# Optimization experiments

Hardware: AMD Instinct MI355X
Metric: run time of the kernel (lower is better)

Reference implementation:

```python
import jax, jax.numpy as jnp
import numpy as np

EPS = 1e-5


def gather_nodes(nodes, idx):
    # nodes: [B,N,C], idx: [B,N,K] -> [B,N,K,C]
    return jax.vmap(lambda n, e: n[e])(nodes, idx)


def layer_norm(x, g, b):
    m = jnp.mean(x, axis=-1, keepdims=True)
    v = jnp.mean((x - m) ** 2, axis=-1, keepdims=True)
    return (x - m) * jax.lax.rsqrt(v + EPS) * g + b


def linear(x, W, b):
    return x @ W + b


def setup_inputs() -> dict:
    key = jax.random.key(0)
    B, N, K, H = 2, 2048, 48, 128
    ks = jax.random.split(key, 32)
    it = iter(range(32))
    def nrm(shape, scale=0.05):
        return jax.random.normal(ks[next(it)], shape, dtype=jnp.float32) * scale
    inp = {
        "h_V": nrm((B, N, H), 1.0),
        "h_V_atom": nrm((B, N, H), 1.0),
        "h_E": nrm((B, N, K, H), 1.0),
        # message MLP 1: in = H + 2*(H+H) = 5H = 640
        "W1": nrm((5 * H, H)), "b1": jnp.zeros((H,), jnp.float32),
        "W2": nrm((H, H)), "b2": jnp.zeros((H,), jnp.float32),
        "W3": nrm((H, H)), "b3": jnp.zeros((H,), jnp.float32),
        # message MLP 2: in = H + (H+H) = 3H = 384
        "W11": nrm((3 * H, H)), "b11": jnp.zeros((H,), jnp.float32),
        "W12": nrm((H, H)), "b12": jnp.zeros((H,), jnp.float32),
        "W13": nrm((H, H)), "b13": jnp.zeros((H,), jnp.float32),
        # FFN
        "W_in": nrm((H, 4 * H)), "b_in": jnp.zeros((4 * H,), jnp.float32),
        "W_out": nrm((4 * H, H)), "b_out": jnp.zeros((H,), jnp.float32),
        # LayerNorms
        "g1": jnp.ones((H,), jnp.float32), "be1": jnp.zeros((H,), jnp.float32),
        "g2": jnp.ones((H,), jnp.float32), "be2": jnp.zeros((H,), jnp.float32),
        "g3": jnp.ones((H,), jnp.float32), "be3": jnp.zeros((H,), jnp.float32),
        "mask_V": jnp.ones((B, N), jnp.float32),
        "mask_attend": jnp.ones((B, N, K), jnp.float32),
        "E_idx": jax.random.randint(ks[next(it)], (B, N, K), 0, N),
    }
    return inp


def reference(h_V, h_V_atom, h_E, W1, b1, W2, b2, W3, b3, W11, b11, W12, b12,
              W13, b13, W_in, b_in, W_out, b_out, g1, be1, g2, be2, g3, be3,
              mask_V, mask_attend, E_idx):
    gelu = lambda x: jax.nn.gelu(x, approximate=False)
    SCALE = 30.0
    K = h_E.shape[-2]

    # --- node message ---
    h_EV = jnp.concatenate([
        jnp.broadcast_to(h_V[:, :, None, :], h_E.shape[:3] + (h_V.shape[-1],)),
        h_E, gather_nodes(h_V, E_idx),
        h_E, gather_nodes(h_V_atom, E_idx),
    ], axis=-1)  # [B,N,K,5H]
    h_message = linear(gelu(linear(gelu(linear(h_EV, W1, b1)), W2, b2)), W3, b3)
    h_message = mask_attend[..., None] * h_message
    dh = jnp.sum(h_message, axis=-2) / SCALE
    h_V = layer_norm(h_V + dh, g1, be1)

    # --- FFN ---
    dh = linear(gelu(linear(h_V, W_in, b_in)), W_out, b_out)
    h_V = layer_norm(h_V + dh, g2, be2)
    h_V = mask_V[..., None] * h_V

    # --- edge update ---
    h_EV2 = jnp.concatenate([
        jnp.broadcast_to(h_V[:, :, None, :], h_E.shape[:3] + (h_V.shape[-1],)),
        h_E, gather_nodes(h_V, E_idx),
    ], axis=-1)  # [B,N,K,3H]
    h_message = linear(gelu(linear(gelu(linear(h_EV2, W11, b11)), W12, b12)), W13, b13)
    h_E = layer_norm(h_E + h_message, g3, be3)
    return (h_V, h_E)
```

## Files before the change

kernel.cpp:

```cpp
#include <hip/hip_runtime.h>
#include <hip/hip_bf16.h>

#define H 128
#define NN 2048
#define BB 2
#define EPSF 1e-5f

typedef __bf16 bf16;
typedef bf16 bf16x8 __attribute__((ext_vector_type(8)));
typedef bf16 bf16x4 __attribute__((ext_vector_type(4)));
typedef float f32x4 __attribute__((ext_vector_type(4)));

#define U1_F     155648
#define U2_F     679936
#define HVMID_F  1204224
#define HVMID_B  3457024
#define HV2_B    3981312
#define HV_B     4505600
#define HVA_B    5029888

__device__ __forceinline__ float gelu_f(float x) {
    float u = x * x;
    float p = __builtin_fmaf(u, 0.044715f, 1.0f);
    float w = x * p;
    float e = __builtin_amdgcn_exp2f(w * -2.3022083f);
    return x * __builtin_amdgcn_rcpf(1.0f + e);
}

#define MFMA16(a, b, c) __builtin_amdgcn_mfma_f32_16x16x32_bf16((a), (b), (c), 0, 0, 0)

#define GEMM_PIPE(U, A_EXPR, B0p, B1p, ACC)                                       \
    {                                                                             \
        bf16x8 bq0[3], bq1[3];                                                    \
        _Pragma("unroll")                                                         \
        for (int j = 0; j < 3 && j < (U); ++j) {                                  \
            bq0[j] = *(const bf16x8*)((B0p) + j * 32);                            \
            bq1[j] = *(const bf16x8*)((B1p) + j * 32);                            \
        }                                                                         \
        bf16x8 afc[3], afn[3];                                                    \
        _Pragma("unroll")                                                         \
        for (int rt = 0; rt < 3; ++rt) { const int u = 0; afc[rt] = (A_EXPR); }   \
        _Pragma("unroll")                                                         \
        for (int uu = 0; uu < (U); ++uu) {                                        \
            if (uu + 1 < (U)) {                                                   \
                _Pragma("unroll")                                                 \
                for (int rt = 0; rt < 3; ++rt) { const int u = uu + 1; afn[rt] = (A_EXPR); } \
            }                                                                     \
            __builtin_amdgcn_s_setprio(1);                                        \
            _Pragma("unroll")                                                     \
            for (int rt = 0; rt < 3; ++rt) {                                      \
                ACC[rt][0] = MFMA16(afc[rt], bq0[uu % 3], ACC[rt][0]);            \
                ACC[rt][1] = MFMA16(afc[rt], bq1[uu % 3], ACC[rt][1]);            \
            }                                                                     \
            __builtin_amdgcn_s_setprio(0);                                        \
            if (uu + 3 < (U)) {                                                   \
                bq0[uu % 3] = *(const bf16x8*)((B0p) + (uu + 3) * 32);            \
                bq1[uu % 3] = *(const bf16x8*)((B1p) + (uu + 3) * 32);            \
            }                                                                     \
            _Pragma("unroll")                                                     \
            for (int rt = 0; rt < 3; ++rt) afc[rt] = afn[rt];                     \
        }                                                                         \
    }

#define PACK_STORE(DST, ROW, PCOL, V0, V1)                                        \
    {                                                                             \
        union { bf16 h[2]; unsigned u; } pk_;                                     \
        pk_.h[0] = (V0); pk_.h[1] = (V1);                                         \
        *(unsigned*)&DST[ROW][PCOL] = pk_.u;                                      \
    }

__global__ void prep_weights(const float* __restrict__ W1, const float* __restrict__ W2,
                             const float* __restrict__ W3, const float* __restrict__ W11,
                             const float* __restrict__ W12, const float* __restrict__ W13,
                             const float* __restrict__ Win, const float* __restrict__ Wout,
                             bf16* __restrict__ ws)
{
    int i = blockIdx.x * 256 + threadIdx.x;
    float v;
    if (i < 65536) {
        int c = i >> 9, k = i & 511, s = k >> 7, k0 = k & 127;
        if (s == 0)      v = W1[k0 * H + c];
        else if (s == 1) v = W1[(128 + k0) * H + c] + W1[(384 + k0) * H + c];
        else if (s == 2) v = W1[(256 + k0) * H + c];
        else             v = W1[(512 + k0) * H + c];
    } else if (i < 81920)  { int j = i - 65536;  int c = j >> 7, p = j & 127;
                             int k = (p & ~31) + ((p & 1) << 4) + ((p & 31) >> 1);
                             v = W2[k * H + c]; }
    else if (i < 98304)    { int j = i - 81920;  int c = j >> 7, p = j & 127;
                             int k = (p & ~31) + ((p & 1) << 4) + ((p & 31) >> 1);
                             v = W3[k * H + c]; }
    else if (i < 147456)   { int j = i - 98304;  int c = j / 384, k = j - c * 384; v = W11[k * H + c]; }
    else if (i < 163840)   { int j = i - 147456; int c = j >> 7, p = j & 127;
                             int k = (p & ~31) + ((p & 1) << 4) + ((p & 31) >> 1);
                             v = W12[k * H + c]; }
    else if (i < 180224)   { int j = i - 163840; int c = j >> 7, p = j & 127;
                             int k = (p & ~31) + ((p & 1) << 4) + ((p & 31) >> 1);
                             v = W13[k * H + c]; }
    else if (i < 245760)   { int j = i - 180224; int jj = j >> 7, k = j & 127; v = Win[k * 512 + jj]; }
    else                   { int j = i - 245760; int c = j >> 9, k = j & 511; v = Wout[k * H + c]; }
    ws[i] = (bf16)v;
}

__global__ __launch_bounds__(512) void u1_kernel(
    const float* __restrict__ hV, const float* __restrict__ hVa,
    const float* __restrict__ b1, bf16* __restrict__ ws, float* __restrict__ wsf)
{
    int n0 = blockIdx.x * 128;
    int t = threadIdx.x, w = t >> 6, l = t & 63, l16 = l & 15, lg = l >> 4;
    int wm = w >> 2, wn = w & 3;
    __shared__ __align__(16) bf16 sA[128][136];

    #pragma unroll
    for (int i = 0; i < 8; ++i) {
        int idx = t + i * 512;
        int row = idx >> 5, c4 = (idx & 31) << 2;
        f32x4 v = *(const f32x4*)(hV + (size_t)(n0 + row) * H + c4);
        bf16x4 o; o[0] = (bf16)v[0]; o[1] = (bf16)v[1]; o[2] = (bf16)v[2]; o[3] = (bf16)v[3];
        *(bf16x4*)(&sA[row][c4]) = o;
        *(bf16x4*)(ws + HV_B + (size_t)(n0 + row) * H + c4) = o;
        f32x4 va = *(const f32x4*)(hVa + (size_t)(n0 + row) * H + c4);
        bf16x4 oa; oa[0] = (bf16)va[0]; oa[1] = (bf16)va[1]; oa[2] = (bf16)va[2]; oa[3] = (bf16)va[3];
        *(bf16x4*)(ws + HVA_B + (size_t)(n0 + row) * H + c4) = oa;
    }
    __syncthreads();

    f32x4 acc[4][2];
    #pragma unroll
    for (int rt = 0; rt < 4; ++rt)
        #pragma unroll
        for (int c2 = 0; c2 < 2; ++c2) acc[rt][c2] = (f32x4){0.f, 0.f, 0.f, 0.f};
    #pragma unroll
    for (int kk = 0; kk < 4; ++kk) {
        bf16x8 af[4];
        #pragma unroll
        for (int rt = 0; rt < 4; ++rt)
            af[rt] = *(const bf16x8*)(&sA[wm * 64 + rt * 16 + l16][kk * 32 + lg * 8]);
        #pragma unroll
        for (int c2 = 0; c2 < 2; ++c2) {
            int c = wn * 32 + c2 * 16 + l16;
            bf16x8 bfr = *(const bf16x8*)(&ws[(size_t)c * 512 + kk * 32 + lg * 8]);
            #pragma unroll
            for (int rt = 0; rt < 4; ++rt)
                acc[rt][c2] = MFMA16(af[rt], bfr, acc[rt][c2]);
        }
    }
    #pragma unroll
    for (int c2 = 0; c2 < 2; ++c2) {
        int col = wn * 32 + c2 * 16 + l16;
        float bb = b1[col];
        #pragma unroll
        for (int rt = 0; rt < 4; ++rt)
            #pragma unroll
            for (int i = 0; i < 4; ++i) {
                int row = wm * 64 + rt * 16 + lg * 4 + i;
                wsf[U1_F + (size_t)(n0 + row) * H + col] = acc[rt][c2][i] + bb;
            }
    }
}

__global__ __launch_bounds__(256, 4) void node_msg_kernel(
    const float* __restrict__ hV, const float* __restrict__ hE,
    const float* __restrict__ b2, const float* __restrict__ b3,
    const float* __restrict__ g1, const float* __restrict__ be1,
    const float* __restrict__ maskA, const int* __restrict__ Eidx,
    bf16* __restrict__ ws, float* __restrict__ wsf)
{
    __shared__ __align__(16) char smem[27136];
    bf16 (*sA)[264]  = (bf16(*)[264])smem;
    bf16 (*sH1)[136] = (bf16(*)[136])smem;
    bf16 (*sH2)[136] = (bf16(*)[136])(smem + 13056);
    float* sDH = (float*)(smem + 26112);

    int n = blockIdx.x, b = n >> 11;
    int t = threadIdx.x, w = t >> 6, l = t & 63, l16 = l & 15, lg = l >> 4;

    int col0 = w * 32 + l16, col1 = col0 + 16;
    int pcol = w * 32 + l16 * 2;
    float u1v0 = wsf[U1_F + (size_t)n * H + col0];
    float u1v1 = wsf[U1_F + (size_t)n * H + col1];
    float b2v0 = b2[col0], b2v1 = b2[col1];
    float b3v0 = b3[col0], b3v1 = b3[col1];

    int r0 = t >> 4, c8g = (t & 15) << 3;
    int nbrv[3];
    #pragma unroll
    for (int i = 0; i < 3; ++i) nbrv[i] = Eidx[n * 48 + r0 + i * 16];

    #pragma unroll
    for (int i = 0; i < 6; ++i) {
        int idx = t + i * 256;
        int row = idx >> 5, c4 = (idx & 31) << 2;
        f32x4 v = *(const f32x4*)(hE + ((size_t)n * 48 + row) * H + c4);
        bf16x4 o; o[0] = (bf16)v[0]; o[1] = (bf16)v[1]; o[2] = (bf16)v[2]; o[3] = (bf16)v[3];
        *(bf16x4*)(&sA[row][c4]) = o;
    }
    bf16x8 gva[3];
    #pragma unroll
    for (int i = 0; i < 3; ++i) {
        int row = r0 + i * 16;
        size_t nb = ((size_t)b * NN + nbrv[i]) * H + c8g;
        *(bf16x8*)(&sA[row][128 + c8g]) = *(const bf16x8*)(ws + HV_B + nb);
        gva[i] = *(const bf16x8*)(ws + HVA_B + nb);
    }
    __syncthreads();

    f32x4 acc[3][2];
    #pragma unroll
    for (int rt = 0; rt < 3; ++rt)
        #pragma unroll
        for (int c2 = 0; c2 < 2; ++c2) acc[rt][c2] = (f32x4){0.f, 0.f, 0.f, 0.f};
    {
        const bf16* B0 = ws + (size_t)col0 * 512 + 128 + lg * 8;
        const bf16* B1 = ws + (size_t)col1 * 512 + 128 + lg * 8;
        GEMM_PIPE(8, (*(const bf16x8*)(&sA[rt * 16 + l16][u * 32 + lg * 8])), B0, B1, acc)
    }
    __syncthreads();

    #pragma unroll
    for (int i = 0; i < 3; ++i)
        *(bf16x8*)(&sA[r0 + i * 16][128 + c8g]) = gva[i];
    __syncthreads();

    {
        const bf16* B0 = ws + (size_t)col0 * 512 + 384 + lg * 8;
        const bf16* B1 = ws + (size_t)col1 * 512 + 384 + lg * 8;
        GEMM_PIPE(4, (*(const bf16x8*)(&sA[rt * 16 + l16][128 + u * 32 + lg * 8])), B0, B1, acc)
    }
    __syncthreads();

    #pragma unroll
    for (int rt = 0; rt < 3; ++rt)
        #pragma unroll
        for (int i = 0; i < 4; ++i) {
            int row = rt * 16 + lg * 4 + i;
            bf16 v0 = (bf16)gelu_f(acc[rt][0][i] + u1v0);
            bf16 v1 = (bf16)gelu_f(acc[rt][1][i] + u1v1);
            PACK_STORE(sH1, row, pcol, v0, v1)
        }
    __syncthreads();

    f32x4 a2[3][2];
    #pragma unroll
    for (int rt = 0; rt < 3; ++rt)
        #pragma unroll
        for (int c2 = 0; c2 < 2; ++c2) a2[rt][c2] = (f32x4){0.f, 0.f, 0.f, 0.f};
    {
        const bf16* B0 = ws + 65536 + (size_t)col0 * 128 + lg * 8;
        const bf16* B1 = ws + 65536 + (size_t)col1 * 128 + lg * 8;
        GEMM_PIPE(4, (*(const bf16x8*)(&sH1[rt * 16 + l16][u * 32 + lg * 8])), B0, B1, a2)
    }
    #pragma unroll
    for (int rt = 0; rt < 3; ++rt)
        #pragma unroll
        for (int i = 0; i < 4; ++i) {
            int row = rt * 16 + lg * 4 + i;
            bf16 v0 = (bf16)gelu_f(a2[rt][0][i] + b2v0);
            bf16 v1 = (bf16)gelu_f(a2[rt][1][i] + b2v1);
            PACK_STORE(sH2, row, pcol, v0, v1)
        }
    __syncthreads();

    float mk[3][4];
    #pragma unroll
    for (int rt = 0; rt < 3; ++rt)
        #pragma unroll
        for (int i = 0; i < 4; ++i)
            mk[rt][i] = maskA[n * 48 + rt * 16 + lg * 4 + i];

    f32x4 a3[3][2];
    #pragma unroll
    for (int rt = 0; rt < 3; ++rt)
        #pragma unroll
        for (int c2 = 0; c2 < 2; ++c2) a3[rt][c2] = (f32x4){0.f, 0.f, 0.f, 0.f};
    {
        const bf16* B0 = ws + 81920 + (size_t)col0 * 128 + lg * 8;
        const bf16* B1 = ws + 81920 + (size_t)col1 * 128 + lg * 8;
        GEMM_PIPE(4, (*(const bf16x8*)(&sH2[rt * 16 + l16][u * 32 + lg * 8])), B0, B1, a3)
    }
    float r0s = 0.f, r1s = 0.f;
    #pragma unroll
    for (int rt = 0; rt < 3; ++rt)
        #pragma unroll
        for (int i = 0; i < 4; ++i) {
            r0s += (a3[rt][0][i] + b3v0) * mk[rt][i];
            r1s += (a3[rt][1][i] + b3v1) * mk[rt][i];
        }
    r0s += __shfl_xor(r0s, 16); r0s += __shfl_xor(r0s, 32);
    r1s += __shfl_xor(r1s, 16); r1s += __shfl_xor(r1s, 32);
    if (l < 16) { sDH[w * 32 + l] = r0s; sDH[w * 32 + 16 + l] = r1s; }
    __syncthreads();

    if (w == 0) {
        float x0 = hV[(size_t)n * H + l] + sDH[l] * (1.0f / 30.0f);
        float x1 = hV[(size_t)n * H + l + 64] + sDH[l + 64] * (1.0f / 30.0f);
        float s1 = x0 + x1, s2 = x0 * x0 + x1 * x1;
        #pragma unroll
        for (int off = 32; off; off >>= 1) { s1 += __shfl_xor(s1, off); s2 += __shfl_xor(s2, off); }
        float m = s1 * (1.f / 128.f);
        float rs = rsqrtf(s2 * (1.f / 128.f) - m * m + EPSF);
        float y0 = (x0 - m) * rs * g1[l] + be1[l];
        float y1 = (x1 - m) * rs * g1[l + 64] + be1[l + 64];
        wsf[HVMID_F + (size_t)n * H + l] = y0;
        wsf[HVMID_F + (size_t)n * H + l + 64] = y1;
        ws[HVMID_B + (size_t)n * H + l] = (bf16)y0;
        ws[HVMID_B + (size_t)n * H + l + 64] = (bf16)y1;
    }
}

__global__ __launch_bounds__(512) void ffn_kernel(
    const float* __restrict__ b_in, const float* __restrict__ b_out,
    const float* __restrict__ b11, const float* __restrict__ g2,
    const float* __restrict__ be2, const float* __restrict__ maskV,
    bf16* __restrict__ ws, float* __restrict__ wsf, float* __restrict__ outV)
{
    int n0 = blockIdx.x * 32;
    int t = threadIdx.x, w = t >> 6, l = t & 63, l16 = l & 15, lg = l >> 4;

    __shared__ __align__(16) char smem[8704 + 33280];
    bf16 (*sA)[136]  = (bf16(*)[136])(smem);
    bf16 (*sFF)[520] = (bf16(*)[520])(smem + 8704);
    float (*sX)[132] = (float(*)[132])(smem + 8704);

    {
        int row = t >> 4, c8 = (t & 15) << 3;
        *(bf16x8*)(&sA[row][c8]) = *(const bf16x8*)(ws + HVMID_B + (size_t)(n0 + row) * H + c8);
    }
    __syncthreads();

    f32x4 a1[2][4];
    #pragma unroll
    for (int rt = 0; rt < 2; ++rt)
        #pragma unroll
        for (int ct = 0; ct < 4; ++ct) a1[rt][ct] = (f32x4){0.f, 0.f, 0.f, 0.f};
    #pragma unroll
    for (int kk = 0; kk < 4; ++kk) {
        bf16x8 af[2];
        #pragma unroll
        for (int rt = 0; rt < 2; ++rt)
            af[rt] = *(const bf16x8*)(&sA[rt * 16 + l16][kk * 32 + lg * 8]);
        #pragma unroll
        for (int ct = 0; ct < 4; ++ct) {
            int c = w * 64 + ct * 16 + l16;
            bf16x8 bfr = *(const bf16x8*)(&ws[180224 + (size_t)c * 128 + kk * 32 + lg * 8]);
            #pragma unroll
            for (int rt = 0; rt < 2; ++rt)
                a1[rt][ct] = MFMA16(af[rt], bfr, a1[rt][ct]);
        }
    }
    #pragma unroll
    for (int ct = 0; ct < 4; ++ct) {
        int c = w * 64 + ct * 16 + l16;
        float bb = b_in[c];
        #pragma unroll
        for (int rt = 0; rt < 2; ++rt)
            #pragma unroll
            for (int i = 0; i < 4; ++i) {
                int row = rt * 16 + lg * 4 + i;
                sFF[row][c] = (bf16)gelu_f(a1[rt][ct][i] + bb);
            }
    }
    __syncthreads();

    f32x4 a2[2];
    a2[0] = (f32x4){0.f, 0.f, 0.f, 0.f}; a2[1] = (f32x4){0.f, 0.f, 0.f, 0.f};
    int cc = w * 16 + l16;
    #pragma unroll
    for (int kk = 0; kk < 16; ++kk) {
        bf16x8 af[2];
        #pragma unroll
        for (int rt = 0; rt < 2; ++rt)
            af[rt] = *(const bf16x8*)(&sFF[rt * 16 + l16][kk * 32 + lg * 8]);
        bf16x8 bfr = *(const bf16x8*)(&ws[245760 + (size_t)cc * 512 + kk * 32 + lg * 8]);
        #pragma unroll
        for (int rt = 0; rt < 2; ++rt)
            a2[rt] = MFMA16(af[rt], bfr, a2[rt]);
    }
    __syncthreads();
    {
        float bb = b_out[cc];
        #pragma unroll
        for (int rt = 0; rt < 2; ++rt)
            #pragma unroll
            for (int i = 0; i < 4; ++i) {
                int row = rt * 16 + lg * 4 + i;
                sX[row][cc] = a2[rt][i] + bb + wsf[HVMID_F + (size_t)(n0 + row) * H + cc];
            }
    }
    __syncthreads();

    if (t < 128) {
        int row = t >> 2, q = t & 3;
        float xr[32], s1 = 0.f, s2 = 0.f;
        #pragma unroll
        for (int j = 0; j < 32; ++j) {
            float x = sX[row][q * 32 + j];
            xr[j] = x; s1 += x; s2 += x * x;
        }
        s1 += __shfl_xor(s1, 1); s1 += __shfl_xor(s1, 2);
        s2 += __shfl_xor(s2, 1); s2 += __shfl_xor(s2, 2);
        float m = s1 * (1.f / 128.f);
        float vv = s2 * (1.f / 128.f) - m * m;
        float rs = rsqrtf(vv + EPSF);
        float mv = maskV[n0 + row];
        #pragma unroll
        for (int j = 0; j < 32; ++j) {
            int c = q * 32 + j;
            float y = ((xr[j] - m) * rs * g2[c] + be2[c]) * mv;
            outV[(size_t)(n0 + row) * H + c] = y;
            ws[HV2_B + (size_t)(n0 + row) * H + c] = (bf16)y;
            sA[row][c] = (bf16)y;
        }
    }
    __syncthreads();

    f32x4 a3[2];
    a3[0] = (f32x4){0.f, 0.f, 0.f, 0.f}; a3[1] = (f32x4){0.f, 0.f, 0.f, 0.f};
    #pragma unroll
    for (int kk = 0; kk < 4; ++kk) {
        bf16x8 af[2];
        #pragma unroll
        for (int rt = 0; rt < 2; ++rt)
            af[rt] = *(const bf16x8*)(&sA[rt * 16 + l16][kk * 32 + lg * 8]);
        bf16x8 bfr = *(const bf16x8*)(&ws[98304 + (size_t)cc * 384 + kk * 32 + lg * 8]);
        #pragma unroll
        for (int rt = 0; rt < 2; ++rt)
            a3[rt] = MFMA16(af[rt], bfr, a3[rt]);
    }
    {
        float bb = b11[cc];
        #pragma unroll
        for (int rt = 0; rt < 2; ++rt)
            #pragma unroll
            for (int i = 0; i < 4; ++i) {
                int row = rt * 16 + lg * 4 + i;
                wsf[U2_F + (size_t)(n0 + row) * H + cc] = a3[rt][i] + bb;
            }
    }
}

__global__ __launch_bounds__(256, 4) void edge_kernel(
    const float* __restrict__ hE, const float* __restrict__ b12,
    const float* __restrict__ b13, const float* __restrict__ g3,
    const float* __restrict__ be3, const int* __restrict__ Eidx,
    const bf16* __restrict__ ws, const float* __restrict__ wsf,
    float* __restrict__ outE)
{
    __shared__ __align__(16) char smem[26112];
    bf16 (*sA)[264]  = (bf16(*)[264])smem;
    bf16 (*sH1)[136] = (bf16(*)[136])smem;
    bf16 (*sH2)[136] = (bf16(*)[136])(smem + 13056);
    float (*sP1)[4]  = (float(*)[4])smem;
    float (*sP2)[4]  = (float(*)[4])(smem + 1024);

    int n = blockIdx.x, b = n >> 11;
    int t = threadIdx.x, w = t >> 6, l = t & 63, l16 = l & 15, lg = l >> 4;

    int col0 = w * 32 + l16, col1 = col0 + 16;
    int pcol = w * 32 + l16 * 2;
    float u2v0 = wsf[U2_F + (size_t)n * H + col0];
    float u2v1 = wsf[U2_F + (size_t)n * H + col1];
    float b12v0 = b12[col0], b12v1 = b12[col1];
    float b13v0 = b13[col0], b13v1 = b13[col1];
    float g3v0 = g3[col0], g3v1 = g3[col1];
    float be3v0 = be3[col0], be3v1 = be3[col1];

    #pragma unroll
    for (int i = 0; i < 6; ++i) {
        int idx = t + i * 256;
        int row = idx >> 5, c4 = (idx & 31) << 2;
        f32x4 v = *(const f32x4*)(hE + ((size_t)n * 48 + row) * H + c4);
        bf16x4 o; o[0] = (bf16)v[0]; o[1] = (bf16)v[1]; o[2] = (bf16)v[2]; o[3] = (bf16)v[3];
        *(bf16x4*)(&sA[row][c4]) = o;
    }
    #pragma unroll
    for (int i = 0; i < 3; ++i) {
        int idx = t + i * 256;
        int row = idx >> 4, c8 = (idx & 15) << 3;
        int nbr = Eidx[n * 48 + row];
        *(bf16x8*)(&sA[row][128 + c8]) =
            *(const bf16x8*)(ws + HV2_B + ((size_t)b * NN + nbr) * H + c8);
    }
    __syncthreads();

    f32x4 acc[3][2];
    #pragma unroll
    for (int rt = 0; rt < 3; ++rt)
        #pragma unroll
        for (int c2 = 0; c2 < 2; ++c2) acc[rt][c2] = (f32x4){0.f, 0.f, 0.f, 0.f};
    {
        const bf16* B0 = ws + 98304 + (size_t)col0 * 384 + 128 + lg * 8;
        const bf16* B1 = ws + 98304 + (size_t)col1 * 384 + 128 + lg * 8;
        GEMM_PIPE(8, (*(const bf16x8*)(&sA[rt * 16 + l16][u * 32 + lg * 8])), B0, B1, acc)
    }

    float rv[3][2][4];
    #pragma unroll
    for (int rt = 0; rt < 3; ++rt)
        #pragma unroll
        for (int c2 = 0; c2 < 2; ++c2)
            #pragma unroll
            for (int i = 0; i < 4; ++i)
                rv[rt][c2][i] = (float)sA[rt * 16 + lg * 4 + i][c2 ? col1 : col0];
    __syncthreads();

    #pragma unroll
    for (int rt = 0; rt < 3; ++rt)
        #pragma unroll
        for (int i = 0; i < 4; ++i) {
            int row = rt * 16 + lg * 4 + i;
            bf16 v0 = (bf16)gelu_f(acc[rt][0][i] + u2v0);
            bf16 v1 = (bf16)gelu_f(acc[rt][1][i] + u2v1);
            PACK_STORE(sH1, row, pcol, v0, v1)
        }
    __syncthreads();

    f32x4 a2[3][2];
    #pragma unroll
    for (int rt = 0; rt < 3; ++rt)
        #pragma unroll
        for (int c2 = 0; c2 < 2; ++c2) a2[rt][c2] = (f32x4){0.f, 0.f, 0.f, 0.f};
    {
        const bf16* B0 = ws + 147456 + (size_t)col0 * 128 + lg * 8;
        const bf16* B1 = ws + 147456 + (size_t)col1 * 128 + lg * 8;
        GEMM_PIPE(4, (*(const bf16x8*)(&sH1[rt * 16 + l16][u * 32 + lg * 8])), B0, B1, a2)
    }
    #pragma unroll
    for (int rt = 0; rt < 3; ++rt)
        #pragma unroll
        for (int i = 0; i < 4; ++i) {
            int row = rt * 16 + lg * 4 + i;
            bf16 v0 = (bf16)gelu_f(a2[rt][0][i] + b12v0);
            bf16 v1 = (bf16)gelu_f(a2[rt][1][i] + b12v1);
            PACK_STORE(sH2, row, pcol, v0, v1)
        }
    __syncthreads();

    f32x4 a3[3][2];
    #pragma unroll
    for (int rt = 0; rt < 3; ++rt)
        #pragma unroll
        for (int c2 = 0; c2 < 2; ++c2) a3[rt][c2] = (f32x4){0.f, 0.f, 0.f, 0.f};
    {
        const bf16* B0 = ws + 163840 + (size_t)col0 * 128 + lg * 8;
        const bf16* B1 = ws + 163840 + (size_t)col1 * 128 + lg * 8;
        GEMM_PIPE(4, (*(const bf16x8*)(&sH2[rt * 16 + l16][u * 32 + lg * 8])), B0, B1, a3)
    }

    float s1r[3][4], s2r[3][4];
    #pragma unroll
    for (int rt = 0; rt < 3; ++rt)
        #pragma unroll
        for (int i = 0; i < 4; ++i) { s1r[rt][i] = 0.f; s2r[rt][i] = 0.f; }
    #pragma unroll
    for (int c2 = 0; c2 < 2; ++c2) {
        float bb = c2 ? b13v1 : b13v0;
        #pragma unroll
        for (int rt = 0; rt < 3; ++rt)
            #pragma unroll
            for (int i = 0; i < 4; ++i) {
                float v = a3[rt][c2][i] + bb + rv[rt][c2][i];
                a3[rt][c2][i] = v;
                s1r[rt][i] += v; s2r[rt][i] += v * v;
            }
    }
    #pragma unroll
    for (int mseg = 1; mseg < 16; mseg <<= 1)
        #pragma unroll
        for (int rt = 0; rt < 3; ++rt)
            #pragma unroll
            for (int i = 0; i < 4; ++i) {
                s1r[rt][i] += __shfl_xor(s1r[rt][i], mseg);
                s2r[rt][i] += __shfl_xor(s2r[rt][i], mseg);
            }
    if (l16 == 0) {
        #pragma unroll
        for (int rt = 0; rt < 3; ++rt)
            #pragma unroll
            for (int i = 0; i < 4; ++i) {
                int row = rt * 16 + lg * 4 + i;
                sP1[row][w] = s1r[rt][i];
                sP2[row][w] = s2r[rt][i];
            }
    }
    __syncthreads();

    #pragma unroll
    for (int rt = 0; rt < 3; ++rt)
        #pragma unroll
        for (int i = 0; i < 4; ++i) {
            int row = rt * 16 + lg * 4 + i;
            f32x4 p1 = *(const f32x4*)sP1[row];
            f32x4 p2 = *(const f32x4*)sP2[row];
            float s1 = p1[0] + p1[1] + p1[2] + p1[3];
            float s2 = p2[0] + p2[1] + p2[2] + p2[3];
            float mn = s1 * (1.f / 128.f);
            float rs = rsqrtf(s2 * (1.f / 128.f) - mn * mn + EPSF);
            size_t rb = ((size_t)n * 48 + row) * H;
            outE[rb + col0] = (a3[rt][0][i] - mn) * rs * g3v0 + be3v0;
            outE[rb + col1] = (a3[rt][1][i] - mn) * rs * g3v1 + be3v1;
        }
}

extern "C" void kernel_launch(void* const* d_in, const int* in_sizes, int n_in,
                              void* d_out, int out_size, void* d_ws, size_t ws_size,
                              hipStream_t stream)
{
    const float* hV    = (const float*)d_in[0];
    const float* hVa   = (const float*)d_in[1];
    const float* hE    = (const float*)d_in[2];
    const float* W1    = (const float*)d_in[3];
    const float* b1    = (const float*)d_in[4];
    const float* W2    = (const float*)d_in[5];
    const float* b2    = (const float*)d_in[6];
    const float* W3    = (const float*)d_in[7];
    const float* b3    = (const float*)d_in[8];
    const float* W11   = (const float*)d_in[9];
    const float* b11   = (const float*)d_in[10];
    const float* W12   = (const float*)d_in[11];
    const float* b12   = (const float*)d_in[12];
    const float* W13   = (const float*)d_in[13];
    const float* b13   = (const float*)d_in[14];
    const float* Win   = (const float*)d_in[15];
    const float* b_in  = (const float*)d_in[16];
    const float* Wout  = (const float*)d_in[17];
    const float* b_out = (const float*)d_in[18];
    const float* g1    = (const float*)d_in[19];
    const float* be1   = (const float*)d_in[20];
    const float* g2    = (const float*)d_in[21];
    const float* be2   = (const float*)d_in[22];
    const float* g3    = (const float*)d_in[23];
    const float* be3   = (const float*)d_in[24];
    const float* maskV = (const float*)d_in[25];
    const float* maskA = (const float*)d_in[26];
    const int*   Eidx  = (const int*)  d_in[27];

    bf16*  ws   = (bf16*)d_ws;
    float* wsf  = (float*)d_ws;
    float* outV = (float*)d_out;
    float* outE = outV + (size_t)BB * NN * H;

    prep_weights<<<1216, 256, 0, stream>>>(W1, W2, W3, W11, W12, W13, Win, Wout, ws);
    u1_kernel<<<32, 512, 0, stream>>>(hV, hVa, b1, ws, wsf);
    node_msg_kernel<<<BB * NN, 256, 0, stream>>>(hV, hE, b2, b3, g1, be1, maskA, Eidx, ws, wsf);
    ffn_kernel<<<BB * NN / 32, 512, 0, stream>>>(b_in, b_out, b11, g2, be2, maskV, ws, wsf, outV);
    edge_kernel<<<BB * NN, 256, 0, stream>>>(hE, b12, b13, g3, be3, Eidx, ws, wsf, outE);
}
```

Measured before the change: 198.1 us.

## Precompute per-node neighbor projections and gather fp32 results instead of features

```diff
diff --git a/kernel.cpp b/kernel.cpp
--- a/kernel.cpp
+++ b/kernel.cpp
@@ -14,10 +14,9 @@
 #define U1_F     155648
 #define U2_F     679936
 #define HVMID_F  1204224
+#define V2_F     1990656
+#define V1_F     2252800
 #define HVMID_B  3457024
-#define HV2_B    3981312
-#define HV_B     4505600
-#define HVA_B    5029888
 
 __device__ __forceinline__ float gelu_f(float x) {
     float u = x * x;
@@ -103,12 +102,13 @@
 
 __global__ __launch_bounds__(512) void u1_kernel(
     const float* __restrict__ hV, const float* __restrict__ hVa,
-    const float* __restrict__ b1, bf16* __restrict__ ws, float* __restrict__ wsf)
+    const float* __restrict__ b1, const bf16* __restrict__ ws, float* __restrict__ wsf)
 {
     int n0 = blockIdx.x * 128;
     int t = threadIdx.x, w = t >> 6, l = t & 63, l16 = l & 15, lg = l >> 4;
     int wm = w >> 2, wn = w & 3;
     __shared__ __align__(16) bf16 sA[128][136];
+    __shared__ __align__(16) bf16 sB[128][136];
 
     #pragma unroll
     for (int i = 0; i < 8; ++i) {
@@ -117,18 +117,20 @@
         f32x4 v = *(const f32x4*)(hV + (size_t)(n0 + row) * H + c4);
         bf16x4 o; o[0] = (bf16)v[0]; o[1] = (bf16)v[1]; o[2] = (bf16)v[2]; o[3] = (bf16)v[3];
         *(bf16x4*)(&sA[row][c4]) = o;
-        *(bf16x4*)(ws + HV_B + (size_t)(n0 + row) * H + c4) = o;
         f32x4 va = *(const f32x4*)(hVa + (size_t)(n0 + row) * H + c4);
         bf16x4 oa; oa[0] = (bf16)va[0]; oa[1] = (bf16)va[1]; oa[2] = (bf16)va[2]; oa[3] = (bf16)va[3];
-        *(bf16x4*)(ws + HVA_B + (size_t)(n0 + row) * H + c4) = oa;
-    }
-    __syncthreads();
-
-    f32x4 acc[4][2];
+        *(bf16x4*)(&sB[row][c4]) = oa;
+    }
+    __syncthreads();
+
+    f32x4 accU[4][2], accV[4][2];
     #pragma unroll
     for (int rt = 0; rt < 4; ++rt)
         #pragma unroll
-        for (int c2 = 0; c2 < 2; ++c2) acc[rt][c2] = (f32x4){0.f, 0.f, 0.f, 0.f};
+        for (int c2 = 0; c2 < 2; ++c2) {
+            accU[rt][c2] = (f32x4){0.f, 0.f, 0.f, 0.f};
+            accV[rt][c2] = (f32x4){0.f, 0.f, 0.f, 0.f};
+        }
     #pragma unroll
     for (int kk = 0; kk < 4; ++kk) {
         bf16x8 af[4];
@@ -138,10 +140,28 @@
         #pragma unroll
         for (int c2 = 0; c2 < 2; ++c2) {
             int c = wn * 32 + c2 * 16 + l16;
-            bf16x8 bfr = *(const bf16x8*)(&ws[(size_t)c * 512 + kk * 32 + lg * 8]);
+            bf16x8 bU = *(const bf16x8*)(&ws[(size_t)c * 512 + kk * 32 + lg * 8]);
+            bf16x8 bV = *(const bf16x8*)(&ws[(size_t)c * 512 + 256 + kk * 32 + lg * 8]);
+            #pragma unroll
+            for (int rt = 0; rt < 4; ++rt) {
+                accU[rt][c2] = MFMA16(af[rt], bU, accU[rt][c2]);
+                accV[rt][c2] = MFMA16(af[rt], bV, accV[rt][c2]);
+            }
+        }
+    }
+    #pragma unroll
+    for (int kk = 0; kk < 4; ++kk) {
+        bf16x8 af[4];
+        #pragma unroll
+        for (int rt = 0; rt < 4; ++rt)
+            af[rt] = *(const bf16x8*)(&sB[wm * 64 + rt * 16 + l16][kk * 32 + lg * 8]);
+        #pragma unroll
+        for (int c2 = 0; c2 < 2; ++c2) {
+            int c = wn * 32 + c2 * 16 + l16;
+            bf16x8 bV = *(const bf16x8*)(&ws[(size_t)c * 512 + 384 + kk * 32 + lg * 8]);
             #pragma unroll
             for (int rt = 0; rt < 4; ++rt)
-                acc[rt][c2] = MFMA16(af[rt], bfr, acc[rt][c2]);
+                accV[rt][c2] = MFMA16(af[rt], bV, accV[rt][c2]);
         }
     }
     #pragma unroll
@@ -153,7 +173,8 @@
             #pragma unroll
             for (int i = 0; i < 4; ++i) {
                 int row = wm * 64 + rt * 16 + lg * 4 + i;
-                wsf[U1_F + (size_t)(n0 + row) * H + col] = acc[rt][c2][i] + bb;
+                wsf[U1_F + (size_t)(n0 + row) * H + col] = accU[rt][c2][i] + bb;
+                wsf[V1_F + (size_t)(n0 + row) * H + col] = accV[rt][c2][i];
             }
     }
 }
@@ -166,7 +187,7 @@
     bf16* __restrict__ ws, float* __restrict__ wsf)
 {
     __shared__ __align__(16) char smem[27136];
-    bf16 (*sA)[264]  = (bf16(*)[264])smem;
+    bf16 (*sA)[136]  = (bf16(*)[136])smem;
     bf16 (*sH1)[136] = (bf16(*)[136])smem;
     bf16 (*sH2)[136] = (bf16(*)[136])(smem + 13056);
     float* sDH = (float*)(smem + 26112);
@@ -181,10 +202,17 @@
     float b2v0 = b2[col0], b2v1 = b2[col1];
     float b3v0 = b3[col0], b3v1 = b3[col1];
 
-    int r0 = t >> 4, c8g = (t & 15) << 3;
-    int nbrv[3];
-    #pragma unroll
-    for (int i = 0; i < 3; ++i) nbrv[i] = Eidx[n * 48 + r0 + i * 16];
+    float v1v0[3][4], v1v1[3][4];
+    #pragma unroll
+    for (int rt = 0; rt < 3; ++rt)
+        #pragma unroll
+        for (int i = 0; i < 4; ++i) {
+            int row = rt * 16 + lg * 4 + i;
+            int nbr = Eidx[n * 48 + row];
+            const float* vp = wsf + V1_F + ((size_t)b * NN + nbr) * H;
+            v1v0[rt][i] = vp[col0];
+            v1v1[rt][i] = vp[col1];
+        }
 
     #pragma unroll
     for (int i = 0; i < 6; ++i) {
@@ -194,14 +222,6 @@
         bf16x4 o; o[0] = (bf16)v[0]; o[1] = (bf16)v[1]; o[2] = (bf16)v[2]; o[3] = (bf16)v[3];
         *(bf16x4*)(&sA[row][c4]) = o;
     }
-    bf16x8 gva[3];
-    #pragma unroll
-    for (int i = 0; i < 3; ++i) {
-        int row = r0 + i * 16;
-        size_t nb = ((size_t)b * NN + nbrv[i]) * H + c8g;
-        *(bf16x8*)(&sA[row][128 + c8g]) = *(const bf16x8*)(ws + HV_B + nb);
-        gva[i] = *(const bf16x8*)(ws + HVA_B + nb);
-    }
     __syncthreads();
 
     f32x4 acc[3][2];
@@ -212,19 +232,7 @@
     {
         const bf16* B0 = ws + (size_t)col0 * 512 + 128 + lg * 8;
         const bf16* B1 = ws + (size_t)col1 * 512 + 128 + lg * 8;
-        GEMM_PIPE(8, (*(const bf16x8*)(&sA[rt * 16 + l16][u * 32 + lg * 8])), B0, B1, acc)
-    }
-    __syncthreads();
-
-    #pragma unroll
-    for (int i = 0; i < 3; ++i)
-        *(bf16x8*)(&sA[r0 + i * 16][128 + c8g]) = gva[i];
-    __syncthreads();
-
-    {
-        const bf16* B0 = ws + (size_t)col0 * 512 + 384 + lg * 8;
-        const bf16* B1 = ws + (size_t)col1 * 512 + 384 + lg * 8;
-        GEMM_PIPE(4, (*(const bf16x8*)(&sA[rt * 16 + l16][128 + u * 32 + lg * 8])), B0, B1, acc)
+        GEMM_PIPE(4, (*(const bf16x8*)(&sA[rt * 16 + l16][u * 32 + lg * 8])), B0, B1, acc)
     }
     __syncthreads();
 
@@ -233,8 +241,8 @@
         #pragma unroll
         for (int i = 0; i < 4; ++i) {
             int row = rt * 16 + lg * 4 + i;
-            bf16 v0 = (bf16)gelu_f(acc[rt][0][i] + u1v0);
-            bf16 v1 = (bf16)gelu_f(acc[rt][1][i] + u1v1);
+            bf16 v0 = (bf16)gelu_f(acc[rt][0][i] + u1v0 + v1v0[rt][i]);
+            bf16 v1 = (bf16)gelu_f(acc[rt][1][i] + u1v1 + v1v1[rt][i]);
             PACK_STORE(sH1, row, pcol, v0, v1)
         }
     __syncthreads();
@@ -407,24 +415,27 @@
             int c = q * 32 + j;
             float y = ((xr[j] - m) * rs * g2[c] + be2[c]) * mv;
             outV[(size_t)(n0 + row) * H + c] = y;
-            ws[HV2_B + (size_t)(n0 + row) * H + c] = (bf16)y;
             sA[row][c] = (bf16)y;
         }
     }
     __syncthreads();
 
-    f32x4 a3[2];
+    f32x4 a3[2], a4[2];
     a3[0] = (f32x4){0.f, 0.f, 0.f, 0.f}; a3[1] = (f32x4){0.f, 0.f, 0.f, 0.f};
+    a4[0] = (f32x4){0.f, 0.f, 0.f, 0.f}; a4[1] = (f32x4){0.f, 0.f, 0.f, 0.f};
     #pragma unroll
     for (int kk = 0; kk < 4; ++kk) {
         bf16x8 af[2];
         #pragma unroll
         for (int rt = 0; rt < 2; ++rt)
             af[rt] = *(const bf16x8*)(&sA[rt * 16 + l16][kk * 32 + lg * 8]);
-        bf16x8 bfr = *(const bf16x8*)(&ws[98304 + (size_t)cc * 384 + kk * 32 + lg * 8]);
-        #pragma unroll
-        for (int rt = 0; rt < 2; ++rt)
-            a3[rt] = MFMA16(af[rt], bfr, a3[rt]);
+        bf16x8 bU = *(const bf16x8*)(&ws[98304 + (size_t)cc * 384 + kk * 32 + lg * 8]);
+        bf16x8 bV = *(const bf16x8*)(&ws[98304 + (size_t)cc * 384 + 256 + kk * 32 + lg * 8]);
+        #pragma unroll
+        for (int rt = 0; rt < 2; ++rt) {
+            a3[rt] = MFMA16(af[rt], bU, a3[rt]);
+            a4[rt] = MFMA16(af[rt], bV, a4[rt]);
+        }
     }
     {
         float bb = b11[cc];
@@ -434,6 +445,7 @@
             for (int i = 0; i < 4; ++i) {
                 int row = rt * 16 + lg * 4 + i;
                 wsf[U2_F + (size_t)(n0 + row) * H + cc] = a3[rt][i] + bb;
+                wsf[V2_F + (size_t)(n0 + row) * H + cc] = a4[rt][i];
             }
     }
 }
@@ -446,7 +458,7 @@
     float* __restrict__ outE)
 {
     __shared__ __align__(16) char smem[26112];
-    bf16 (*sA)[264]  = (bf16(*)[264])smem;
+    bf16 (*sA)[136]  = (bf16(*)[136])smem;
     bf16 (*sH1)[136] = (bf16(*)[136])smem;
     bf16 (*sH2)[136] = (bf16(*)[136])(smem + 13056);
     float (*sP1)[4]  = (float(*)[4])smem;
@@ -464,6 +476,18 @@
     float g3v0 = g3[col0], g3v1 = g3[col1];
     float be3v0 = be3[col0], be3v1 = be3[col1];
 
+    float v2v0[3][4], v2v1[3][4];
+    #pragma unroll
+    for (int rt = 0; rt < 3; ++rt)
+        #pragma unroll
+        for (int i = 0; i < 4; ++i) {
+            int row = rt * 16 + lg * 4 + i;
+            int nbr = Eidx[n * 48 + row];
+            const float* vp = wsf + V2_F + ((size_t)b * NN + nbr) * H;
+            v2v0[rt][i] = vp[col0];
+            v2v1[rt][i] = vp[col1];
+        }
+
     #pragma unroll
     for (int i = 0; i < 6; ++i) {
         int idx = t + i * 256;
@@ -472,14 +496,6 @@
         bf16x4 o; o[0] = (bf16)v[0]; o[1] = (bf16)v[1]; o[2] = (bf16)v[2]; o[3] = (bf16)v[3];
         *(bf16x4*)(&sA[row][c4]) = o;
     }
-    #pragma unroll
-    for (int i = 0; i < 3; ++i) {
-        int idx = t + i * 256;
-        int row = idx >> 4, c8 = (idx & 15) << 3;
-        int nbr = Eidx[n * 48 + row];
-        *(bf16x8*)(&sA[row][128 + c8]) =
-            *(const bf16x8*)(ws + HV2_B + ((size_t)b * NN + nbr) * H + c8);
-    }
     __syncthreads();
 
     f32x4 acc[3][2];
@@ -490,7 +506,7 @@
     {
         const bf16* B0 = ws + 98304 + (size_t)col0 * 384 + 128 + lg * 8;
         const bf16* B1 = ws + 98304 + (size_t)col1 * 384 + 128 + lg * 8;
-        GEMM_PIPE(8, (*(const bf16x8*)(&sA[rt * 16 + l16][u * 32 + lg * 8])), B0, B1, acc)
+        GEMM_PIPE(4, (*(const bf16x8*)(&sA[rt * 16 + l16][u * 32 + lg * 8])), B0, B1, acc)
     }
 
     float rv[3][2][4];
@@ -508,8 +524,8 @@
         #pragma unroll
         for (int i = 0; i < 4; ++i) {
             int row = rt * 16 + lg * 4 + i;
-            bf16 v0 = (bf16)gelu_f(acc[rt][0][i] + u2v0);
-            bf16 v1 = (bf16)gelu_f(acc[rt][1][i] + u2v1);
+            bf16 v0 = (bf16)gelu_f(acc[rt][0][i] + u2v0 + v2v0[rt][i]);
+            bf16 v1 = (bf16)gelu_f(acc[rt][1][i] + u2v1 + v2v1[rt][i]);
             PACK_STORE(sH1, row, pcol, v0, v1)
         }
     __syncthreads();
```

Measured after the change: 174.5 us (median of 2 runs). 11.9% less time.
